# Kernel tuning notes

Hardware: AMD Instinct MI355X
Metric: run time of the kernel (lower is better)

Reference implementation:

```python
import jax, jax.numpy as jnp
import numpy as np
import math

B, T, E, H = 4, 4096, 1024, 16
D = E // H  # head dim
EPS_DENOM = 1e-6
LN_EPS = 1e-5


def setup_inputs() -> dict:
    key = jax.random.key(0)
    ks = jax.random.split(key, 8)
    s = 0.02
    return {
        "x": jax.random.normal(ks[0], (B, T, E), jnp.float32),
        "ln1_w": jnp.ones((E,), jnp.float32),
        "ln1_b": jnp.zeros((E,), jnp.float32),
        "wq": jax.random.normal(ks[1], (E, E), jnp.float32) * s,
        "bq": jnp.zeros((E,), jnp.float32),
        "wk": jax.random.normal(ks[2], (E, E), jnp.float32) * s,
        "bk": jnp.zeros((E,), jnp.float32),
        "wv": jax.random.normal(ks[3], (E, E), jnp.float32) * s,
        "bv": jnp.zeros((E,), jnp.float32),
        "wo": jax.random.normal(ks[4], (E, E), jnp.float32) * s,
        "bo": jnp.zeros((E,), jnp.float32),
        "ln2_w": jnp.ones((E,), jnp.float32),
        "ln2_b": jnp.zeros((E,), jnp.float32),
        "w_fc": jax.random.normal(ks[5], (E, 4 * E), jnp.float32) * s,
        "b_fc": jnp.zeros((4 * E,), jnp.float32),
        "w_proj": jax.random.normal(ks[6], (4 * E, E), jnp.float32) * s,
        "b_proj": jnp.zeros((E,), jnp.float32),
    }


def _layernorm(x, w, b):
    mu = jnp.mean(x, axis=-1, keepdims=True)
    var = jnp.mean(jnp.square(x - mu), axis=-1, keepdims=True)
    return (x - mu) * jax.lax.rsqrt(var + LN_EPS) * w + b


def _cosformer_attn(x, wq, bq, wk, bk, wv, bv, wo, bo):
    # ReLU feature map on q, k projections
    q = jax.nn.relu(x @ wq + bq)  # [B,T,E]
    k = jax.nn.relu(x @ wk + bk)
    v = x @ wv + bv
    # split heads -> [B,H,T,D]
    q = q.reshape(B, T, H, D).transpose(0, 2, 1, 3)
    k = k.reshape(B, T, H, D).transpose(0, 2, 1, 3)
    v = v.reshape(B, T, H, D).transpose(0, 2, 1, 3)
    # cosine reweighting: idx_i = pi/2 * (i+1)/M, M = T (self-attention)
    idx = (math.pi / 2.0) * jnp.arange(1, T + 1, dtype=x.dtype) / T  # [T]
    s = jnp.sin(idx)[None, None, :, None]
    c = jnp.cos(idx)[None, None, :, None]
    q_ = jnp.concatenate([q * s, q * c], axis=-1)  # [B,H,T,2D]
    k_ = jnp.concatenate([k * s, k * c], axis=-1)  # [B,H,T,2D]
    # non-causal linear attention: O = Q' (K'^T V) / (Q' K'^T 1)
    kv = jnp.einsum("bhtd,bhte->bhde", k_, v)       # [B,H,2D,D]
    z = 1.0 / jnp.maximum(jnp.einsum("bhtd,bhd->bht", q_, k_.sum(axis=2)), EPS_DENOM)
    out = jnp.einsum("bhtd,bhde,bht->bhte", q_, kv, z)  # [B,H,T,D]
    out = out.transpose(0, 2, 1, 3).reshape(B, T, E)
    return out @ wo + bo


def reference(x, ln1_w, ln1_b, wq, bq, wk, bk, wv, bv, wo, bo,
              ln2_w, ln2_b, w_fc, b_fc, w_proj, b_proj):
    h = _layernorm(x, ln1_w, ln1_b)
    x = x + _cosformer_attn(h, wq, bq, wk, bk, wv, bv, wo, bo)
    h = _layernorm(x, ln2_w, ln2_b)
    h = jax.nn.gelu(h @ w_fc + b_fc, approximate=False) @ w_proj + b_proj
    return x + h
```

## Files before the change

### kernel.cpp

```cpp
#include <hip/hip_runtime.h>

#define PI_F 3.14159265358979f
#define MT 16384
#define EE 1024
#define FF 4096
#define NCH 8
#define CHT (4096 / NCH)

typedef unsigned short u16;
typedef __attribute__((ext_vector_type(8))) short short8;
typedef __attribute__((ext_vector_type(4))) float f32x4;

__device__ __forceinline__ float bf2f(u16 u) {
  unsigned int v = ((unsigned int)u) << 16;
  float f;
  __builtin_memcpy(&f, &v, 4);
  return f;
}
__device__ __forceinline__ u16 f2bf(float f) {
  unsigned int x;
  __builtin_memcpy(&x, &f, 4);
  unsigned int r = x + 0x7fffu + ((x >> 16) & 1u);
  return (u16)(r >> 16);
}
__device__ __forceinline__ float ldin(const void* p, long i, int f32) {
  return f32 ? ((const float*)p)[i] : bf2f(((const u16*)p)[i]);
}
__device__ __forceinline__ void async16(const u16* g, u16* l) {
  __builtin_amdgcn_global_load_lds(
      (const __attribute__((address_space(1))) unsigned int*)g,
      (__attribute__((address_space(3))) unsigned int*)l, 16, 0, 0);
}

__global__ __launch_bounds__(256) void detect_dtype(const u16* __restrict__ x,
                                                    int* __restrict__ flag) {
  const int tid = threadIdx.x;
  int cnt = 0;
  for (int i = tid; i < 2048; i += 256) {
    const int e = (x[i] >> 7) & 0xFF;
    if (e == 0 || e >= 0x90) cnt++;
  }
#pragma unroll
  for (int o = 32; o > 0; o >>= 1) cnt += __shfl_xor(cnt, o);
  __shared__ int s[4];
  if ((tid & 63) == 0) s[tid >> 6] = cnt;
  __syncthreads();
  if (tid == 0) flag[0] = (s[0] + s[1] + s[2] + s[3] > 200) ? 1 : 0;
}

__global__ __launch_bounds__(256) void transpose_in(
    const void* __restrict__ src, const int* __restrict__ flag,
    u16* __restrict__ dst, int R, int C) {
  __shared__ float tile[64][65];
  const int f = *flag;
  const int tx = threadIdx.x & 63, ty = threadIdx.x >> 6;
  const long c0 = (long)blockIdx.x * 64, r0 = (long)blockIdx.y * 64;
#pragma unroll
  for (int i = 0; i < 16; i++) {
    const int r = ty + i * 4;
    tile[r][tx] = ldin(src, (r0 + r) * (long)C + c0 + tx, f);
  }
  __syncthreads();
#pragma unroll
  for (int i = 0; i < 16; i++) {
    const int cc = ty + i * 4;
    dst[(c0 + cc) * (long)R + r0 + tx] = f2bf(tile[tx][cc]);
  }
}

__global__ __launch_bounds__(256) void concat3(
    const void* __restrict__ a, const void* __restrict__ b,
    const void* __restrict__ c, const int* __restrict__ flag,
    float* __restrict__ out) {
  const int i = blockIdx.x * 256 + threadIdx.x;
  const int fl = *flag;
  if (i < 1024) out[i] = ldin(a, i, fl);
  else if (i < 2048) out[i] = ldin(b, i - 1024, fl);
  else if (i < 3072) out[i] = ldin(c, i - 2048, fl);
}

__global__ __launch_bounds__(256) void ln_kernel(
    const void* __restrict__ xin, int xmode, const int* __restrict__ flag,
    const void* __restrict__ w, const void* __restrict__ b,
    u16* __restrict__ out) {
  const long row = blockIdx.x;
  const int tid = threadIdx.x;
  const int fl = *flag;
  const int xf = (xmode == 2) ? fl : xmode;
  float v[4];
  if (xf) {
    const float4 q = ((const float4*)((const float*)xin + row * EE))[tid];
    v[0] = q.x; v[1] = q.y; v[2] = q.z; v[3] = q.w;
  } else {
    const ushort4 u = ((const ushort4*)((const u16*)xin + row * EE))[tid];
    v[0] = bf2f(u.x); v[1] = bf2f(u.y); v[2] = bf2f(u.z); v[3] = bf2f(u.w);
  }
  float sum = v[0] + v[1] + v[2] + v[3];
  float sq = v[0] * v[0] + v[1] * v[1] + v[2] * v[2] + v[3] * v[3];
#pragma unroll
  for (int o = 32; o > 0; o >>= 1) {
    sum += __shfl_xor(sum, o);
    sq += __shfl_xor(sq, o);
  }
  __shared__ float s1[4], s2[4];
  const int wave = tid >> 6, lane = tid & 63;
  if (lane == 0) { s1[wave] = sum; s2[wave] = sq; }
  __syncthreads();
  sum = s1[0] + s1[1] + s1[2] + s1[3];
  sq = s2[0] + s2[1] + s2[2] + s2[3];
  const float mu = sum * (1.f / EE);
  const float var = sq * (1.f / EE) - mu * mu;
  const float rs = rsqrtf(var + 1e-5f);
  ushort4 o4;
  float r0 = (v[0] - mu) * rs * ldin(w, tid * 4 + 0, fl) + ldin(b, tid * 4 + 0, fl);
  float r1 = (v[1] - mu) * rs * ldin(w, tid * 4 + 1, fl) + ldin(b, tid * 4 + 1, fl);
  float r2 = (v[2] - mu) * rs * ldin(w, tid * 4 + 2, fl) + ldin(b, tid * 4 + 2, fl);
  float r3 = (v[3] - mu) * rs * ldin(w, tid * 4 + 3, fl) + ldin(b, tid * 4 + 3, fl);
  o4.x = f2bf(r0); o4.y = f2bf(r1); o4.z = f2bf(r2); o4.w = f2bf(r3);
  ((ushort4*)(out + row * EE))[tid] = o4;
}

__global__ __launch_bounds__(256, 3) void gemm_bf16(
    const u16* __restrict__ A, const u16* __restrict__ Bt,
    const void* __restrict__ bias, int biasF32,
    const void* __restrict__ res, int resMode,
    void* __restrict__ Cout, void* __restrict__ Cv, int outMode, long coff,
    const int* __restrict__ flag, int M, int N, int K, int act) {
  __shared__ u16 As[3][4096];
  __shared__ u16 Bs[3][4096];
  const int tid = threadIdx.x;
  const int lane = tid & 63;
  const int wave = tid >> 6;
  const int quad = lane >> 4;
  const int l16 = lane & 15;
  const int wm = (wave >> 1) * 64;
  const int wn = (wave & 1) * 64;
  const int bid0 = blockIdx.x + gridDim.x * blockIdx.y;
  const int gy = gridDim.y;
  const int width = 8 * gy;
  const int group = bid0 / width;
  const int rem = bid0 - group * width;
  const int bx = group * 8 + (rem & 7);
  const int by = rem >> 3;
  const long bm = (long)bx * 128;
  const long bn = (long)by * 128;

  f32x4 acc[4][4];
#pragma unroll
  for (int i = 0; i < 4; i++)
#pragma unroll
    for (int j = 0; j < 4; j++)
#pragma unroll
      for (int r = 0; r < 4; r++) acc[i][j][r] = 0.f;

  const int trow = tid >> 2;
  const int tswz = (tid & 3) ^ (trow & 3);
  const u16* Ap = A + (bm + trow) * (long)K + tswz * 8;
  const u16* Bp = Bt + (bn + trow) * (long)K + tswz * 8;
  const long rowK64 = 64 * (long)K;

  auto stage = [&](int buf, long kt) {
    u16* Ad = &As[buf][wave * 512];
    u16* Bd = &Bs[buf][wave * 512];
    async16(Ap + kt, Ad);
    async16(Ap + rowK64 + kt, Ad + 2048);
    async16(Bp + kt, Bd);
    async16(Bp + rowK64 + kt, Bd + 2048);
  };
  const int rswz = (quad ^ (l16 & 3)) * 8;
  auto compute = [&](int buf) {
    short8 af[4], bfr[4];
#pragma unroll
    for (int i = 0; i < 4; i++)
      af[i] = *(const short8*)&As[buf][(wm + i * 16 + l16) * 32 + rswz];
#pragma unroll
    for (int i = 0; i < 4; i++)
      bfr[i] = *(const short8*)&Bs[buf][(wn + i * 16 + l16) * 32 + rswz];
    __builtin_amdgcn_s_setprio(1);
#pragma unroll
    for (int mi = 0; mi < 4; mi++)
#pragma unroll
      for (int ni = 0; ni < 4; ni++)
        acc[mi][ni] = __builtin_amdgcn_mfma_f32_16x16x32_bf16(
            af[mi], bfr[ni], acc[mi][ni], 0, 0, 0);
    __builtin_amdgcn_s_setprio(0);
  };

  const int nt = K >> 5;
  stage(0, 0);
  stage(1, 32);
  asm volatile("s_waitcnt vmcnt(4)" ::: "memory");
  __builtin_amdgcn_s_barrier();
  int cb = 0, sb = 2;
  for (int t = 0; t < nt; ++t) {
    const long ts = (t + 2 < nt) ? (long)(t + 2) * 32 : (long)(nt - 1) * 32;
    stage(sb, ts);
    compute(cb);
    asm volatile("s_waitcnt vmcnt(4)" ::: "memory");
    __builtin_amdgcn_s_barrier();
    cb = (cb == 2) ? 0 : cb + 1;
    sb = (sb == 2) ? 0 : sb + 1;
  }
  __syncthreads();

  const int fl = *flag;
  const long Nl = N;
  float bv4[4];
  long gcA[4];
#pragma unroll
  for (int ni = 0; ni < 4; ni++) {
    gcA[ni] = bn + wn + ni * 16 + l16;
    bv4[ni] = biasF32 ? ((const float*)bias)[gcA[ni]] : ldin(bias, gcA[ni], fl);
  }
#pragma unroll
  for (int mi = 0; mi < 4; mi++)
#pragma unroll
    for (int ni = 0; ni < 4; ni++)
#pragma unroll
      for (int r = 0; r < 4; r++) {
        float v = acc[mi][ni][r] + bv4[ni];
        if (act == 1 || (act == 3 && gcA[ni] < 2048)) v = fmaxf(v, 0.f);
        else if (act == 2) v = 0.5f * v * (1.f + erff(v * 0.70710678118654752f));
        acc[mi][ni][r] = v;
      }
  float* sf = (float*)&As[0][0] + wave * 1088;
  const int er = lane >> 2;
  const int ec = (lane & 3) * 16;
#pragma unroll
  for (int mi = 0; mi < 4; mi++) {
#pragma unroll
    for (int ni = 0; ni < 4; ni++)
#pragma unroll
      for (int r = 0; r < 4; r++)
        sf[(quad * 4 + r) * 68 + ni * 16 + l16] = acc[mi][ni][r];
    f32x4 w0 = *(const f32x4*)&sf[er * 68 + ec + 0];
    f32x4 w1 = *(const f32x4*)&sf[er * 68 + ec + 4];
    f32x4 w2 = *(const f32x4*)&sf[er * 68 + ec + 8];
    f32x4 w3 = *(const f32x4*)&sf[er * 68 + ec + 12];
    const long gr = bm + wm + mi * 16 + er;
    const long gc0 = bn + wn + ec;
    const long ib = gr * Nl + gc0;
    if (resMode == 1 || (resMode == 2 && fl)) {
      const f32x4* rp = (const f32x4*)((const float*)res + ib);
      f32x4 r0 = rp[0], r1 = rp[1], r2 = rp[2], r3 = rp[3];
#pragma unroll
      for (int j = 0; j < 4; j++) {
        w0[j] += r0[j]; w1[j] += r1[j]; w2[j] += r2[j]; w3[j] += r3[j];
      }
    } else if (resMode == 2) {
      const short8* rp = (const short8*)((const u16*)res + ib);
      short8 ra = rp[0], rb = rp[1];
#pragma unroll
      for (int j = 0; j < 4; j++) {
        w0[j] += bf2f((u16)ra[j]);
        w1[j] += bf2f((u16)ra[j + 4]);
        w2[j] += bf2f((u16)rb[j]);
        w3[j] += bf2f((u16)rb[j + 4]);
      }
    }
    if (outMode == 1 || (outMode == 2 && fl)) {
      f32x4* op = (f32x4*)((float*)Cout + coff + ib);
      op[0] = w0; op[1] = w1; op[2] = w2; op[3] = w3;
    } else {
      u16 tmp[16];
#pragma unroll
      for (int j = 0; j < 4; j++) {
        tmp[j] = f2bf(w0[j]);
        tmp[j + 4] = f2bf(w1[j]);
        tmp[j + 8] = f2bf(w2[j]);
        tmp[j + 12] = f2bf(w3[j]);
      }
      u16* op;
      if (outMode == 3) {
        const int plane = (int)(bn >> 10);
        u16* dst = (plane == 2) ? (u16*)Cv
                                : ((u16*)Cout + plane * ((long)M << 10));
        op = dst + (gr << 10) + (gc0 & 1023);
      } else {
        op = (u16*)Cout + coff + ib;
      }
      *(short8*)op = *(short8*)&tmp[0];
      *(short8*)(op + 8) = *(short8*)&tmp[8];
    }
  }
}

__global__ __launch_bounds__(256) void kv_partial(
    const u16* __restrict__ k, const u16* __restrict__ v,
    float* __restrict__ kvpart, float* __restrict__ kspart) {
  const int bh = blockIdx.x;
  const int ch = blockIdx.y;
  const int b = bh >> 4, h = bh & 15;
  const int tid = threadIdx.x;
  __shared__ float kl[8][64], vl[8][64];
  const int dkq = tid >> 4;
  const int dvq = tid & 15;
  float accS[4][4] = {}, accC[4][4] = {};
  float ksS[4] = {}, ksC[4] = {};
  const int tt = tid >> 5;
  const int cc = (tid & 31) * 2;
  const long base = ((long)b * 4096 + ch * CHT) * EE + h * 64;
  for (int tb = 0; tb < CHT; tb += 8) {
    const long roff = base + (long)(tb + tt) * EE + cc;
    const unsigned int ku = *(const unsigned int*)(k + roff);
    const unsigned int vu = *(const unsigned int*)(v + roff);
    __syncthreads();
    kl[tt][cc] = bf2f((u16)ku);
    kl[tt][cc + 1] = bf2f((u16)(ku >> 16));
    vl[tt][cc] = bf2f((u16)vu);
    vl[tt][cc + 1] = bf2f((u16)(vu >> 16));
    __syncthreads();
#pragma unroll
    for (int j = 0; j < 8; j++) {
      const int t = ch * CHT + tb + j;
      float s, c;
      __sincosf((float)(t + 1) * (PI_F * 0.5f / 4096.f), &s, &c);
      float kk[4], vv[4];
#pragma unroll
      for (int i = 0; i < 4; i++) {
        kk[i] = kl[j][dkq * 4 + i];
        vv[i] = vl[j][dvq * 4 + i];
      }
#pragma unroll
      for (int i = 0; i < 4; i++) {
        const float ks_ = kk[i] * s, kc_ = kk[i] * c;
        ksS[i] += ks_;
        ksC[i] += kc_;
#pragma unroll
        for (int jj = 0; jj < 4; jj++) {
          accS[i][jj] += ks_ * vv[jj];
          accC[i][jj] += kc_ * vv[jj];
        }
      }
    }
  }
  float* outS = kvpart + (((long)ch * 64 + bh) * 2 + 0) * 4096;
  float* outC = outS + 4096;
#pragma unroll
  for (int i = 0; i < 4; i++)
#pragma unroll
    for (int jj = 0; jj < 4; jj++) {
      outS[(dkq * 4 + i) * 64 + dvq * 4 + jj] = accS[i][jj];
      outC[(dkq * 4 + i) * 64 + dvq * 4 + jj] = accC[i][jj];
    }
  if (dvq == 0) {
    float* oS = kspart + ((long)ch * 64 + bh) * 2 * 64;
#pragma unroll
    for (int i = 0; i < 4; i++) {
      oS[dkq * 4 + i] = ksS[i];
      oS[64 + dkq * 4 + i] = ksC[i];
    }
  }
}

__global__ __launch_bounds__(256) void kv_reduce(
    const float* __restrict__ kvpart, const float* __restrict__ kspart,
    float* __restrict__ kvcomb, float* __restrict__ kscomb) {
  const long KVTOT = 64L * 2 * 4096;
  const long KSTOT = 64L * 2 * 64;
  const long idx = (long)blockIdx.x * 256 + threadIdx.x;
  if (idx < KVTOT) {
    float s = 0.f;
#pragma unroll
    for (int chn = 0; chn < NCH; chn++) s += kvpart[chn * KVTOT + idx];
    kvcomb[idx] = s;
  } else {
    const long i2 = idx - KVTOT;
    if (i2 < KSTOT) {
      float s = 0.f;
#pragma unroll
      for (int chn = 0; chn < NCH; chn++) s += kspart[chn * KSTOT + i2];
      kscomb[i2] = s;
    }
  }
}

__global__ __launch_bounds__(256) void attn_apply(
    const u16* __restrict__ q, const float* __restrict__ kvcomb,
    const float* __restrict__ kscomb, u16* __restrict__ attn) {
  const int bh = blockIdx.x;
  const int b = bh >> 4, h = bh & 15;
  const int t0 = blockIdx.y * 64;
  const int tid = threadIdx.x;
  __shared__ float kvl[2][64][64];
  __shared__ float ksl[2][64];
  __shared__ float ql[64][66];

  const float4* kvsrc = (const float4*)(kvcomb + (long)bh * 8192);
  float4* kvdst = (float4*)&kvl[0][0][0];
#pragma unroll
  for (int i = 0; i < 8; i++) kvdst[tid + 256 * i] = kvsrc[tid + 256 * i];
  if (tid < 32) ((float4*)&ksl[0][0])[tid] = ((const float4*)(kscomb + (long)bh * 128))[tid];
  {
    const int r = tid >> 2;
    const int c = (tid & 3) * 16;
    const u16* qp = q + ((long)b * 4096 + t0 + r) * EE + h * 64 + c;
    const uint4 u0 = *(const uint4*)qp;
    const uint4 u1 = *(const uint4*)(qp + 8);
    unsigned int uu[8] = {u0.x, u0.y, u0.z, u0.w, u1.x, u1.y, u1.z, u1.w};
#pragma unroll
    for (int i = 0; i < 8; i++) {
      ql[r][c + 2 * i] = bf2f((u16)uu[i]);
      ql[r][c + 2 * i + 1] = bf2f((u16)(uu[i] >> 16));
    }
  }
  __syncthreads();

  const int tg = tid >> 4;
  const int dvq = tid & 15;
  const int dv0 = dvq * 4;

  float o1[4][4] = {}, o2[4][4] = {}, zs[4] = {}, zc[4] = {};
  for (int dk = 0; dk < 64; dk++) {
    const float ks0 = ksl[0][dk], ks1 = ksl[1][dk];
    float kv0[4], kv1[4];
#pragma unroll
    for (int j = 0; j < 4; j++) {
      kv0[j] = kvl[0][dk][dv0 + j];
      kv1[j] = kvl[1][dk][dv0 + j];
    }
#pragma unroll
    for (int it = 0; it < 4; it++) {
      const float qv = ql[tg + it * 16][dk];
      zs[it] += qv * ks0;
      zc[it] += qv * ks1;
#pragma unroll
      for (int j = 0; j < 4; j++) {
        o1[it][j] += qv * kv0[j];
        o2[it][j] += qv * kv1[j];
      }
    }
  }
#pragma unroll
  for (int it = 0; it < 4; it++) {
    const int t = t0 + tg + it * 16;
    float s, c;
    __sincosf((float)(t + 1) * (PI_F * 0.5f / 4096.f), &s, &c);
    const float z = s * zs[it] + c * zc[it];
    const float zinv = 1.f / fmaxf(z, 1e-6f);
    ushort4 o4;
    o4.x = f2bf((s * o1[it][0] + c * o2[it][0]) * zinv);
    o4.y = f2bf((s * o1[it][1] + c * o2[it][1]) * zinv);
    o4.z = f2bf((s * o1[it][2] + c * o2[it][2]) * zinv);
    o4.w = f2bf((s * o1[it][3] + c * o2[it][3]) * zinv);
    *(ushort4*)(attn + ((long)b * 4096 + t) * EE + h * 64 + dv0) = o4;
  }
}

extern "C" void kernel_launch(void* const* d_in, const int* in_sizes, int n_in,
                              void* d_out, int out_size, void* d_ws, size_t ws_size,
                              hipStream_t stream) {
  const void* x = d_in[0];
  const void* ln1w = d_in[1];
  const void* ln1b = d_in[2];
  const void* wq = d_in[3];
  const void* bq = d_in[4];
  const void* wk = d_in[5];
  const void* bk = d_in[6];
  const void* wv = d_in[7];
  const void* bv = d_in[8];
  const void* wo = d_in[9];
  const void* bo = d_in[10];
  const void* ln2w = d_in[11];
  const void* ln2b = d_in[12];
  const void* wfc = d_in[13];
  const void* bfc = d_in[14];
  const void* wproj = d_in[15];
  const void* bproj = d_in[16];

  char* ws = (char*)d_ws;
  size_t off = 0;
  auto alloc = [&](size_t bytes) -> char* {
    char* p = ws + off;
    off += (bytes + 255) & ~((size_t)255);
    return p;
  };
  int* flag = (int*)alloc(256);
  u16* wqkvT = (u16*)alloc((size_t)3 * EE * EE * 2);
  u16* woT = (u16*)alloc((size_t)EE * EE * 2);
  u16* wfcT = (u16*)alloc((size_t)EE * FF * 2);
  u16* wprojT = (u16*)alloc((size_t)FF * EE * 2);
  float* qkvBias = (float*)alloc(3072 * 4);
  u16* h = (u16*)alloc((size_t)MT * EE * 2);
  float* x2 = (float*)alloc((size_t)MT * EE * 4);
  u16* qk2 = (u16*)alloc((size_t)2 * MT * EE * 2);
  float* kvpart = (float*)alloc((size_t)NCH * 64 * 2 * 64 * 64 * 4);
  float* kspart = (float*)alloc((size_t)NCH * 64 * 2 * 64 * 4);
  float* kvcomb = (float*)alloc((size_t)64 * 2 * 64 * 64 * 4);
  float* kscomb = (float*)alloc((size_t)64 * 2 * 64 * 4);
  const long PL = (long)MT * EE;
  u16* qb = qk2;
  u16* kb = qk2 + PL;
  u16* vb = (u16*)x2;
  u16* attnb = kb;
  u16* g = qk2;
  (void)ws_size; (void)in_sizes; (void)n_in; (void)out_size;

  detect_dtype<<<1, 256, 0, stream>>>((const u16*)x, flag);

  transpose_in<<<dim3(16, 16), 256, 0, stream>>>(wq, flag, wqkvT, EE, EE);
  transpose_in<<<dim3(16, 16), 256, 0, stream>>>(wk, flag, wqkvT + (size_t)EE * EE, EE, EE);
  transpose_in<<<dim3(16, 16), 256, 0, stream>>>(wv, flag, wqkvT + (size_t)2 * EE * EE, EE, EE);
  transpose_in<<<dim3(16, 16), 256, 0, stream>>>(wo, flag, woT, EE, EE);
  transpose_in<<<dim3(64, 16), 256, 0, stream>>>(wfc, flag, wfcT, EE, FF);
  transpose_in<<<dim3(16, 64), 256, 0, stream>>>(wproj, flag, wprojT, FF, EE);
  concat3<<<12, 256, 0, stream>>>(bq, bk, bv, flag, qkvBias);

  ln_kernel<<<MT, 256, 0, stream>>>(x, 2, flag, ln1w, ln1b, h);

  gemm_bf16<<<dim3(128, 24), 256, 0, stream>>>(h, wqkvT, qkvBias, 1, nullptr, 0,
                                               qk2, vb, 3, 0, flag, MT, 3072, EE, 3);

  kv_partial<<<dim3(64, NCH), 256, 0, stream>>>(kb, vb, kvpart, kspart);
  kv_reduce<<<2080, 256, 0, stream>>>(kvpart, kspart, kvcomb, kscomb);
  attn_apply<<<dim3(64, 64), 256, 0, stream>>>(qb, kvcomb, kscomb, attnb);

  gemm_bf16<<<dim3(128, 8), 256, 0, stream>>>(attnb, woT, bo, 0, x, 2, x2, nullptr,
                                              1, 0, flag, MT, EE, EE, 0);
  ln_kernel<<<MT, 256, 0, stream>>>(x2, 1, flag, ln2w, ln2b, h);

  for (int c = 0; c < 2; c++) {
    const long ro = (long)c * 8192 * EE;
    gemm_bf16<<<dim3(64, 32), 256, 0, stream>>>(h + ro, wfcT, bfc, 0, nullptr, 0,
                                                g, nullptr, 0, 0, flag, 8192, FF, EE, 2);
    gemm_bf16<<<dim3(64, 8), 256, 0, stream>>>(g, wprojT, bproj, 0, x2 + ro, 1,
                                               d_out, nullptr, 2, ro, flag, 8192, EE, FF, 0);
  }
}
```

Measured before the change: 1.131 ms.

## Add 256x256-tile 8-wave GEMM with interleaved staging for QKV, out-proj, FC

```diff
diff --git a/kernel.cpp b/kernel.cpp
--- a/kernel.cpp
+++ b/kernel.cpp
@@ -118,6 +118,186 @@
   float r3 = (v[3] - mu) * rs * ldin(w, tid * 4 + 3, fl) + ldin(b, tid * 4 + 3, fl);
   o4.x = f2bf(r0); o4.y = f2bf(r1); o4.z = f2bf(r2); o4.w = f2bf(r3);
   ((ushort4*)(out + row * EE))[tid] = o4;
+}
+
+__global__ __launch_bounds__(512, 2) void gemm256(
+    const u16* __restrict__ A, const u16* __restrict__ Bt,
+    const void* __restrict__ bias, int biasF32,
+    const void* __restrict__ res, int resMode,
+    void* __restrict__ Cout, void* __restrict__ Cv, int outMode, long coff,
+    const int* __restrict__ flag, int M, int N, int K, int act) {
+  __shared__ u16 As[3][2][4096];
+  __shared__ u16 Bs[3][2][4096];
+  const int tid = threadIdx.x;
+  const int lane = tid & 63;
+  const int wave = tid >> 6;
+  const int wr = wave >> 2;
+  const int wc = wave & 3;
+  const int quad = lane >> 4;
+  const int l16 = lane & 15;
+  const int bid0 = blockIdx.x + gridDim.x * blockIdx.y;
+  const int width = 4 * gridDim.y;
+  const int group = bid0 / width;
+  const int rem = bid0 - group * width;
+  const int bx = group * 4 + (rem & 3);
+  const int by = rem >> 2;
+  const long bm = (long)bx * 256;
+  const long bn = (long)by * 256;
+
+  f32x4 acc[8][4];
+#pragma unroll
+  for (int i = 0; i < 8; i++)
+#pragma unroll
+    for (int j = 0; j < 4; j++)
+#pragma unroll
+      for (int r = 0; r < 4; r++) acc[i][j][r] = 0.f;
+
+  const int sr = tid >> 2;
+  const int su = tid & 3;
+  const u16* Ap = A + (bm + sr) * (long)K + su * 8;
+  const u16* Bp = Bt + (bn + sr) * (long)K + su * 8;
+  const long half128 = 128 * (long)K;
+
+  auto stgA = [&](int d, int h, long kt) {
+    async16(Ap + h * half128 + kt, &As[d][h][0] + wave * 512);
+  };
+  auto stgB = [&](int d, int h, long kt) {
+    async16(Bp + h * half128 + kt, &Bs[d][h][0] + wave * 512);
+  };
+
+  const int nt = K >> 5;
+  stgA(0, 0, 0); stgA(0, 1, 0); stgB(0, 0, 0); stgB(0, 1, 0);
+  stgA(1, 0, 32); stgA(1, 1, 32); stgB(1, 0, 32); stgB(1, 1, 32);
+  asm volatile("s_waitcnt vmcnt(4)" ::: "memory");
+  __builtin_amdgcn_s_barrier();
+
+  int d = 0;
+  for (int t = 0; t < nt; ++t) {
+    const int sd = (t + 2) % 3;
+    const long skt = ((t + 2 < nt) ? (long)(t + 2) : (long)(nt - 1)) * 32;
+    const u16* Ah = &As[d][wr][0];
+    short8 af[4], bfr[4];
+#pragma unroll
+    for (int i = 0; i < 4; i++)
+      af[i] = *(const short8*)&Ah[(i * 16 + l16) * 32 + quad * 8];
+#pragma unroll
+    for (int ni = 0; ni < 4; ni++) {
+      const int cl = wc * 64 + ni * 16 + l16;
+      bfr[ni] = *(const short8*)&Bs[d][cl >> 7][(cl & 127) * 32 + quad * 8];
+    }
+    stgA(sd, 0, skt);
+    stgA(sd, 1, skt);
+    asm volatile("s_waitcnt vmcnt(4)" ::: "memory");
+    __builtin_amdgcn_s_barrier();
+    __builtin_amdgcn_s_setprio(1);
+#pragma unroll
+    for (int mi = 0; mi < 4; mi++)
+#pragma unroll
+      for (int ni = 0; ni < 4; ni++)
+        acc[mi][ni] = __builtin_amdgcn_mfma_f32_16x16x32_bf16(
+            af[mi], bfr[ni], acc[mi][ni], 0, 0, 0);
+    __builtin_amdgcn_s_setprio(0);
+    __builtin_amdgcn_s_barrier();
+#pragma unroll
+    for (int i = 0; i < 4; i++)
+      af[i] = *(const short8*)&Ah[(64 + i * 16 + l16) * 32 + quad * 8];
+    stgB(sd, 0, skt);
+    stgB(sd, 1, skt);
+    asm volatile("s_waitcnt vmcnt(4)" ::: "memory");
+    __builtin_amdgcn_s_barrier();
+    __builtin_amdgcn_s_setprio(1);
+#pragma unroll
+    for (int mi = 0; mi < 4; mi++)
+#pragma unroll
+      for (int ni = 0; ni < 4; ni++)
+        acc[4 + mi][ni] = __builtin_amdgcn_mfma_f32_16x16x32_bf16(
+            af[mi], bfr[ni], acc[4 + mi][ni], 0, 0, 0);
+    __builtin_amdgcn_s_setprio(0);
+    __builtin_amdgcn_s_barrier();
+    d = (d == 2) ? 0 : d + 1;
+  }
+  __syncthreads();
+
+  const int fl = *flag;
+  const long Nl = N;
+  float bv4[4];
+  long gcA[4];
+#pragma unroll
+  for (int ni = 0; ni < 4; ni++) {
+    gcA[ni] = bn + wc * 64 + ni * 16 + l16;
+    bv4[ni] = biasF32 ? ((const float*)bias)[gcA[ni]] : ldin(bias, gcA[ni], fl);
+  }
+#pragma unroll
+  for (int mi = 0; mi < 8; mi++)
+#pragma unroll
+    for (int ni = 0; ni < 4; ni++)
+#pragma unroll
+      for (int r = 0; r < 4; r++) {
+        float v = acc[mi][ni][r] + bv4[ni];
+        if (act == 1 || (act == 3 && gcA[ni] < 2048)) v = fmaxf(v, 0.f);
+        else if (act == 2) v = 0.5f * v * (1.f + erff(v * 0.70710678118654752f));
+        acc[mi][ni][r] = v;
+      }
+  float* sf = (float*)&As[0][0][0] + wave * 1088;
+  const int er = lane >> 2;
+  const int ec = (lane & 3) * 16;
+#pragma unroll
+  for (int mi = 0; mi < 8; mi++) {
+#pragma unroll
+    for (int ni = 0; ni < 4; ni++)
+#pragma unroll
+      for (int r = 0; r < 4; r++)
+        sf[(quad * 4 + r) * 68 + ni * 16 + l16] = acc[mi][ni][r];
+    f32x4 w0 = *(const f32x4*)&sf[er * 68 + ec + 0];
+    f32x4 w1 = *(const f32x4*)&sf[er * 68 + ec + 4];
+    f32x4 w2 = *(const f32x4*)&sf[er * 68 + ec + 8];
+    f32x4 w3 = *(const f32x4*)&sf[er * 68 + ec + 12];
+    const long gr = bm + wr * 128 + mi * 16 + er;
+    const long gc0 = bn + wc * 64 + ec;
+    const long ib = gr * Nl + gc0;
+    if (resMode == 1 || (resMode == 2 && fl)) {
+      const f32x4* rp = (const f32x4*)((const float*)res + ib);
+      f32x4 r0 = rp[0], r1 = rp[1], r2 = rp[2], r3 = rp[3];
+#pragma unroll
+      for (int j = 0; j < 4; j++) {
+        w0[j] += r0[j]; w1[j] += r1[j]; w2[j] += r2[j]; w3[j] += r3[j];
+      }
+    } else if (resMode == 2) {
+      const short8* rp = (const short8*)((const u16*)res + ib);
+      short8 ra = rp[0], rb = rp[1];
+#pragma unroll
+      for (int j = 0; j < 4; j++) {
+        w0[j] += bf2f((u16)ra[j]);
+        w1[j] += bf2f((u16)ra[j + 4]);
+        w2[j] += bf2f((u16)rb[j]);
+        w3[j] += bf2f((u16)rb[j + 4]);
+      }
+    }
+    if (outMode == 1 || (outMode == 2 && fl)) {
+      f32x4* op = (f32x4*)((float*)Cout + coff + ib);
+      op[0] = w0; op[1] = w1; op[2] = w2; op[3] = w3;
+    } else {
+      u16 tmp[16];
+#pragma unroll
+      for (int j = 0; j < 4; j++) {
+        tmp[j] = f2bf(w0[j]);
+        tmp[j + 4] = f2bf(w1[j]);
+        tmp[j + 8] = f2bf(w2[j]);
+        tmp[j + 12] = f2bf(w3[j]);
+      }
+      u16* op;
+      if (outMode == 3) {
+        const int plane = (int)(gc0 >> 10);
+        u16* dst = (plane == 2) ? (u16*)Cv
+                                : ((u16*)Cout + plane * ((long)M << 10));
+        op = dst + (gr << 10) + (gc0 & 1023);
+      } else {
+        op = (u16*)Cout + coff + ib;
+      }
+      *(short8*)op = *(short8*)&tmp[0];
+      *(short8*)(op + 8) = *(short8*)&tmp[8];
+    }
+  }
 }
 
 __global__ __launch_bounds__(256, 3) void gemm_bf16(
@@ -508,21 +688,21 @@
 
   ln_kernel<<<MT, 256, 0, stream>>>(x, 2, flag, ln1w, ln1b, h);
 
-  gemm_bf16<<<dim3(128, 24), 256, 0, stream>>>(h, wqkvT, qkvBias, 1, nullptr, 0,
-                                               qk2, vb, 3, 0, flag, MT, 3072, EE, 3);
+  gemm256<<<dim3(64, 12), 512, 0, stream>>>(h, wqkvT, qkvBias, 1, nullptr, 0,
+                                            qk2, vb, 3, 0, flag, MT, 3072, EE, 3);
 
   kv_partial<<<dim3(64, NCH), 256, 0, stream>>>(kb, vb, kvpart, kspart);
   kv_reduce<<<2080, 256, 0, stream>>>(kvpart, kspart, kvcomb, kscomb);
   attn_apply<<<dim3(64, 64), 256, 0, stream>>>(qb, kvcomb, kscomb, attnb);
 
-  gemm_bf16<<<dim3(128, 8), 256, 0, stream>>>(attnb, woT, bo, 0, x, 2, x2, nullptr,
-                                              1, 0, flag, MT, EE, EE, 0);
+  gemm256<<<dim3(64, 4), 512, 0, stream>>>(attnb, woT, bo, 0, x, 2, x2, nullptr,
+                                           1, 0, flag, MT, EE, EE, 0);
   ln_kernel<<<MT, 256, 0, stream>>>(x2, 1, flag, ln2w, ln2b, h);
 
   for (int c = 0; c < 2; c++) {
     const long ro = (long)c * 8192 * EE;
-    gemm_bf16<<<dim3(64, 32), 256, 0, stream>>>(h + ro, wfcT, bfc, 0, nullptr, 0,
-                                                g, nullptr, 0, 0, flag, 8192, FF, EE, 2);
+    gemm256<<<dim3(32, 16), 512, 0, stream>>>(h + ro, wfcT, bfc, 0, nullptr, 0,
+                                              g, nullptr, 0, 0, flag, 8192, FF, EE, 2);
     gemm_bf16<<<dim3(64, 8), 256, 0, stream>>>(g, wprojT, bproj, 0, x2 + ro, 1,
                                                d_out, nullptr, 2, ro, flag, 8192, EE, FF, 0);
   }
```

Measured after the change: 1.148 ms. Within noise of the previous version (+1.4%).
